# Performance work log

Measured on AMD Instinct MI355X. Metric: run time of the kernel, lower is better.

The kernel has to match this reference:

```python
import jax, jax.numpy as jnp
import numpy as np

D = 1024
H = 16
DH = D // H  # 64
B, S = 4, 1024


def setup_inputs() -> dict:
    key = jax.random.key(0)
    ks = jax.random.split(key, 7)
    sequences = jax.random.normal(ks[0], (B, S, D), dtype=jnp.float32)
    scale = 1.0 / np.sqrt(DH)
    Wq = jax.random.normal(ks[1], (H, DH, DH), dtype=jnp.float32) * scale
    Wk = jax.random.normal(ks[2], (H, DH, DH), dtype=jnp.float32) * scale
    Wv = jax.random.normal(ks[3], (H, DH, DH), dtype=jnp.float32) * scale
    bq = jax.random.normal(ks[4], (H, DH), dtype=jnp.float32) * 0.01
    bk = jax.random.normal(ks[5], (H, DH), dtype=jnp.float32) * 0.01
    bv = jax.random.normal(ks[6], (H, DH), dtype=jnp.float32) * 0.01
    return {"sequences": sequences, "Wq": Wq, "Wk": Wk, "Wv": Wv,
            "bq": bq, "bk": bk, "bv": bv}


def reference(sequences, Wq, Wk, Wv, bq, bk, bv):
    b, s, d = sequences.shape
    x = sequences.reshape(b, s, H, DH)  # split channels into heads
    # per-head Linear: y = x @ W.T + b (torch convention)
    q = jnp.einsum('bshd,hed->bshe', x, Wq) + bq
    k = jnp.einsum('bshd,hed->bshe', x, Wk) + bk
    v = jnp.einsum('bshd,hed->bshe', x, Wv) + bv
    inv_sqrt_dh = jnp.asarray(1.0 / np.sqrt(DH), dtype=sequences.dtype)
    scores = jnp.einsum('bshe,bthe->bhst', q, k) * inv_sqrt_dh  # [B,H,S,S]
    attn = jax.nn.softmax(scores, axis=-1)
    out = jnp.einsum('bhst,bthe->bshe', attn, v)  # [B,S,H,DH]
    return out.reshape(b, s, d)  # hstack of heads == reshape here
```

## Files before the change

kernel.cpp:

```cpp
#include <hip/hip_runtime.h>

#define H 16
#define DH 64
#define BB 4
#define SS 1024
#define DD 1024

typedef __attribute__((ext_vector_type(8))) short bf16x8;
typedef __attribute__((ext_vector_type(4))) float f32x4;
typedef __attribute__((ext_vector_type(4))) unsigned int u32x4;
typedef _Float16 f16x4 __attribute__((ext_vector_type(4)));
typedef _Float16 f16x8 __attribute__((ext_vector_type(8)));
typedef __fp16 hf16x2 __attribute__((ext_vector_type(2)));

#define QSCALE 0.18033688011112042f

#if __has_builtin(__builtin_amdgcn_exp2f)
__device__ __forceinline__ float fast_exp2(float x) {
    return __builtin_amdgcn_exp2f(x);
}
#else
__device__ __forceinline__ float fast_exp2(float x) {
    float r;
    asm("v_exp_f32 %0, %1" : "=v"(r) : "v"(x));
    return r;
}
#endif

__device__ __forceinline__ unsigned short f2bf(float f) {
    union { float f; unsigned u; } v; v.f = f;
    unsigned u = v.u;
    return (unsigned short)((u + 0x7FFFu + ((u >> 16) & 1u)) >> 16);
}

__device__ __forceinline__ unsigned short f2h(float f) {
    union { _Float16 h; unsigned short u; } v;
    v.h = (_Float16)f;
    return v.u;
}

__device__ __forceinline__ void pack8(unsigned short* dst, f32x4 a, f32x4 b) {
    unsigned u0 = (unsigned)f2bf(a[0]) | ((unsigned)f2bf(a[1]) << 16);
    unsigned u1 = (unsigned)f2bf(a[2]) | ((unsigned)f2bf(a[3]) << 16);
    unsigned u2 = (unsigned)f2bf(b[0]) | ((unsigned)f2bf(b[1]) << 16);
    unsigned u3 = (unsigned)f2bf(b[2]) | ((unsigned)f2bf(b[3]) << 16);
    u32x4 v = {u0, u1, u2, u3};
    *(u32x4*)dst = v;
}

__device__ __forceinline__ void async_cp1k(const unsigned short* g,
                                           unsigned short* l, int lane) {
    __builtin_amdgcn_global_load_lds(
        (const __attribute__((address_space(1))) unsigned int*)(g + lane * 8),
        (__attribute__((address_space(3))) unsigned int*)l, 16, 0, 0);
}

__global__ __launch_bounds__(256) void wprep_kernel(
    const float* __restrict__ Wq, const float* __restrict__ Wk,
    const float* __restrict__ Wv, unsigned short* __restrict__ Wp)
{
    const int tg = blockIdx.x * 256 + threadIdx.x;
    const int r = tg >> 2, part = tg & 3;
    const int e = r & 63, hm = r >> 6;
    const int m = hm % 3, h = hm / 3;
    const float* src = (m == 0 ? Wq : (m == 1 ? Wk : Wv)) +
                       (size_t)(h * 64 + e) * 64 + part * 16;
    const float scale = (m == 0) ? QSCALE : 1.0f;
    f32x4 f0 = ((const f32x4*)src)[0];
    f32x4 f1 = ((const f32x4*)src)[1];
    f32x4 f2 = ((const f32x4*)src)[2];
    f32x4 f3 = ((const f32x4*)src)[3];
    f0 *= scale; f1 *= scale; f2 *= scale; f3 *= scale;
    unsigned short tmp[16];
    pack8(tmp, f0, f1);
    pack8(tmp + 8, f2, f3);
    unsigned short* dst = Wp + (size_t)(hm * 64 + e) * 64;
    const int c0 = part * 2, sw = e & 7;
    *(u32x4*)(dst + (c0 ^ sw) * 8)       = *(const u32x4*)tmp;
    *(u32x4*)(dst + ((c0 + 1) ^ sw) * 8) = *(const u32x4*)(tmp + 8);
}

__global__ __launch_bounds__(256) void qkv_kernel(
    const float* __restrict__ x, const unsigned short* __restrict__ Wp,
    const float* __restrict__ bq, const float* __restrict__ bk,
    const float* __restrict__ bv,
    unsigned short* __restrict__ Qg, unsigned short* __restrict__ Kg,
    unsigned short* __restrict__ VTg)
{
    __shared__ __align__(16) unsigned short Xl[4096];
    __shared__ __align__(16) unsigned short Wl[12288];

    const int bid = blockIdx.x;
    const int sc = bid & 15, h = (bid >> 4) & 15, b = bid >> 8;
    const int s0 = sc * 64;
    const int tid = threadIdx.x;
    const int lane = tid & 63, w = tid >> 6;

    {
        const unsigned short* wbase = Wp + (size_t)h * 12288;
#pragma unroll
        for (int sub = 0; sub < 6; sub++) {
            const int off = w * 3072 + sub * 512;
            async_cp1k(wbase + off, &Wl[off], lane);
        }
    }
    {
        const int s = tid >> 2, part = tid & 3;
        const float* src = x + ((size_t)(b * SS + s0 + s)) * DD + h * DH + part * 16;
        f32x4 f0 = ((const f32x4*)src)[0];
        f32x4 f1 = ((const f32x4*)src)[1];
        f32x4 f2 = ((const f32x4*)src)[2];
        f32x4 f3 = ((const f32x4*)src)[3];
        unsigned short tmp[16];
        pack8(tmp, f0, f1);
        pack8(tmp + 8, f2, f3);
        const int c0 = part * 2, sws = s & 7;
        *(u32x4*)&Xl[s * 64 + (c0 ^ sws) * 8]       = *(const u32x4*)tmp;
        *(u32x4*)&Xl[s * 64 + ((c0 + 1) ^ sws) * 8] = *(const u32x4*)(tmp + 8);
    }
    __syncthreads();

    const int l15 = lane & 15, quad = lane >> 4, sw = l15 & 7;

    f32x4 acc[3][4];
#pragma unroll
    for (int m = 0; m < 3; m++)
#pragma unroll
        for (int nt = 0; nt < 4; nt++) acc[m][nt] = (f32x4){0.f, 0.f, 0.f, 0.f};

#pragma unroll
    for (int k2 = 0; k2 < 2; k2++) {
        const int csw = (((k2 << 2) | quad) ^ sw) * 8;
        bf16x8 a = *(const bf16x8*)&Xl[(w * 16 + l15) * 64 + csw];
#pragma unroll
        for (int nt = 0; nt < 4; nt++) {
            const int boff = (nt * 16 + l15) * 64 + csw;
            bf16x8 b0 = *(const bf16x8*)&Wl[boff];
            acc[0][nt] = __builtin_amdgcn_mfma_f32_16x16x32_bf16(a, b0, acc[0][nt], 0, 0, 0);
            bf16x8 b1 = *(const bf16x8*)&Wl[4096 + boff];
            acc[1][nt] = __builtin_amdgcn_mfma_f32_16x16x32_bf16(a, b1, acc[1][nt], 0, 0, 0);
            bf16x8 b2 = *(const bf16x8*)&Wl[8192 + boff];
            acc[2][nt] = __builtin_amdgcn_mfma_f32_16x16x32_bf16(a, b2, acc[2][nt], 0, 0, 0);
        }
    }
    __syncthreads();

#pragma unroll
    for (int nt = 0; nt < 4; nt++) {
        const int e = nt * 16 + l15;
        const float bqs = bq[h * DH + e] * QSCALE;
        const float bks = bk[h * DH + e];
        const float bvs = bv[h * DH + e];
#pragma unroll
        for (int r = 0; r < 4; r++) {
            const int srow = w * 16 + quad * 4 + r;
            Xl[srow * 64 + e] = f2bf(acc[0][nt][r] + bqs);
            Wl[srow * 64 + e] = f2bf(acc[1][nt][r] + bks);
            Wl[4096 + e * 64 + quad * 16 + w * 4 + r] = f2h(acc[2][nt][r] + bvs);
        }
    }
    __syncthreads();
    {
        const size_t bh = (size_t)(b * H + h);
        const int row = tid >> 2, part = tid & 3;
        const int cg = part * 16, c0 = part * 2, swr = row & 7;
        unsigned short* qdst = Qg + (bh * SS + s0 + row) * DH + cg;
        *(u32x4*)qdst       = *(const u32x4*)&Xl[row * 64 + cg];
        *(u32x4*)(qdst + 8) = *(const u32x4*)&Xl[row * 64 + cg + 8];
        unsigned short* kbase = Kg + (bh * 16 + sc) * 4096 + row * 64;
        *(u32x4*)(kbase + (c0 ^ swr) * 8)       = *(const u32x4*)&Wl[row * 64 + c0 * 8];
        *(u32x4*)(kbase + ((c0 + 1) ^ swr) * 8) = *(const u32x4*)&Wl[row * 64 + c0 * 8 + 8];
        unsigned short* vbase = VTg + (bh * 16 + sc) * 4096 + row * 64;
        *(u32x4*)(vbase + (c0 ^ swr) * 8)       = *(const u32x4*)&Wl[4096 + row * 64 + c0 * 8];
        *(u32x4*)(vbase + ((c0 + 1) ^ swr) * 8) = *(const u32x4*)&Wl[4096 + row * 64 + c0 * 8 + 8];
    }
}

__global__ __launch_bounds__(256) void attn_kernel(
    const unsigned short* __restrict__ Qg, const unsigned short* __restrict__ Kg,
    const unsigned short* __restrict__ VTg, float* __restrict__ out)
{
    __shared__ __align__(16) unsigned short Kl0[4096], Kl1[4096];
    __shared__ __align__(16) unsigned short Vl0[4096], Vl1[4096];

    const int bid = blockIdx.x;
    const int bh = bid & 63, qt = bid >> 6;
    const int h = bh & 15, b = bh >> 4;
    const int tid = threadIdx.x;
    const int lane = tid & 63, w = tid >> 6;
    const int l15 = lane & 15, quad = lane >> 4, sw = l15 & 7;

    const unsigned short* Kt = Kg + (size_t)bh * 16 * 4096;
    const unsigned short* Vt = VTg + (size_t)bh * 16 * 4096;

    const int kb0 = l15 * 64 + ((quad)     ^ sw) * 8;
    const int kb1 = l15 * 64 + ((4 | quad) ^ sw) * 8;
    const int vb0 = l15 * 64 + (((quad << 1))     ^ sw) * 8;
    const int vb1 = l15 * 64 + (((quad << 1) | 1) ^ sw) * 8;

    bf16x8 aQ0, aQ1;
    {
        const int qrow = qt * 64 + w * 16 + l15;
        const unsigned short* qp = Qg + ((size_t)bh * SS + qrow) * DH + quad * 8;
        aQ0 = *(const bf16x8*)(qp);
        aQ1 = *(const bf16x8*)(qp + 32);
    }

    {
        const int off = w * 1024;
        async_cp1k(Kt + off,       Kl0 + off,       lane);
        async_cp1k(Kt + off + 512, Kl0 + off + 512, lane);
        async_cp1k(Vt + off,       Vl0 + off,       lane);
        async_cp1k(Vt + off + 512, Vl0 + off + 512, lane);
    }

    f32x4 accO[4];
#pragma unroll
    for (int et = 0; et < 4; et++) accO[et] = (f32x4){0.f, 0.f, 0.f, 0.f};
    float rs_acc = 0.f;

    auto step = [&](int kt, const unsigned short* Kc, const unsigned short* Vc,
                    unsigned short* Kn, unsigned short* Vn) {
        __syncthreads();
        if (kt < 15) {
            const unsigned short* kg = Kt + (kt + 1) * 4096;
            const unsigned short* vg = Vt + (kt + 1) * 4096;
            const int off = w * 1024;
            async_cp1k(kg + off,       Kn + off,       lane);
            async_cp1k(kg + off + 512, Kn + off + 512, lane);
            async_cp1k(vg + off,       Vn + off,       lane);
            async_cp1k(vg + off + 512, Vn + off + 512, lane);
        }

        bf16x8 aK[4][2];
#pragma unroll
        for (int nt = 0; nt < 4; nt++) {
            aK[nt][0] = *(const bf16x8*)(Kc + kb0 + nt * 1024);
            aK[nt][1] = *(const bf16x8*)(Kc + kb1 + nt * 1024);
        }
        f16x8 aV01[4], aV23[4];
#pragma unroll
        for (int et = 0; et < 4; et++) {
            aV01[et] = *(const f16x8*)(Vc + vb0 + et * 1024);
            aV23[et] = *(const f16x8*)(Vc + vb1 + et * 1024);
        }

        f32x4 sc[4];
#pragma unroll
        for (int nt = 0; nt < 4; nt++) {
            f32x4 z = {0.f, 0.f, 0.f, 0.f};
            z = __builtin_amdgcn_mfma_f32_16x16x32_bf16(aK[nt][0], aQ0, z, 0, 0, 0);
            z = __builtin_amdgcn_mfma_f32_16x16x32_bf16(aK[nt][1], aQ1, z, 0, 0, 0);
            sc[nt] = z;
        }

        float rs = 0.f;
        f16x4 pf[4];
#pragma unroll
        for (int nt = 0; nt < 4; nt++) {
            float p0 = fast_exp2(sc[nt][0]);
            float p1 = fast_exp2(sc[nt][1]);
            float p2 = fast_exp2(sc[nt][2]);
            float p3 = fast_exp2(sc[nt][3]);
            rs += (p0 + p1) + (p2 + p3);
            union { hf16x2 h; unsigned u; } lo, hi;
            lo.h = __builtin_amdgcn_cvt_pkrtz(p0, p1);
            hi.h = __builtin_amdgcn_cvt_pkrtz(p2, p3);
            union { unsigned u[2]; f16x4 v; } pk;
            pk.u[0] = lo.u; pk.u[1] = hi.u;
            pf[nt] = pk.v;
        }
        rs_acc += rs;

#pragma unroll
        for (int et = 0; et < 4; et++) {
            f16x4 v0 = __builtin_shufflevector(aV01[et], aV01[et], 0, 1, 2, 3);
            f16x4 v1 = __builtin_shufflevector(aV01[et], aV01[et], 4, 5, 6, 7);
            f16x4 v2 = __builtin_shufflevector(aV23[et], aV23[et], 0, 1, 2, 3);
            f16x4 v3 = __builtin_shufflevector(aV23[et], aV23[et], 4, 5, 6, 7);
            accO[et] = __builtin_amdgcn_mfma_f32_16x16x16f16(v0, pf[0], accO[et], 0, 0, 0);
            accO[et] = __builtin_amdgcn_mfma_f32_16x16x16f16(v1, pf[1], accO[et], 0, 0, 0);
            accO[et] = __builtin_amdgcn_mfma_f32_16x16x16f16(v2, pf[2], accO[et], 0, 0, 0);
            accO[et] = __builtin_amdgcn_mfma_f32_16x16x16f16(v3, pf[3], accO[et], 0, 0, 0);
        }
    };

    for (int i = 0; i < 8; i++) {
        step(2 * i,     Kl0, Vl0, Kl1, Vl1);
        step(2 * i + 1, Kl1, Vl1, Kl0, Vl0);
    }

    {
        float rs = rs_acc;
        rs += __shfl_xor(rs, 16);
        rs += __shfl_xor(rs, 32);
        const float inv = 1.0f / rs;
        const int srow = qt * 64 + w * 16 + l15;
        float* op = out + ((size_t)b * SS + srow) * DD + h * DH;
#pragma unroll
        for (int et = 0; et < 4; et++) {
            f32x4 v = accO[et] * inv;
            *(f32x4*)(op + et * 16 + quad * 4) = v;
        }
    }
}

extern "C" void kernel_launch(void* const* d_in, const int* in_sizes, int n_in,
                              void* d_out, int out_size, void* d_ws, size_t ws_size,
                              hipStream_t stream) {
    const float* x  = (const float*)d_in[0];
    const float* Wq = (const float*)d_in[1];
    const float* Wk = (const float*)d_in[2];
    const float* Wv = (const float*)d_in[3];
    const float* bq = (const float*)d_in[4];
    const float* bk = (const float*)d_in[5];
    const float* bv = (const float*)d_in[6];

    const size_t NE = (size_t)BB * H * SS * DH;
    unsigned short* Qg  = (unsigned short*)d_ws;
    unsigned short* Kg  = Qg + NE;
    unsigned short* VTg = Kg + NE;
    unsigned short* Wp  = VTg + NE;

    wprep_kernel<<<48, 256, 0, stream>>>(Wq, Wk, Wv, Wp);
    qkv_kernel<<<BB * H * (SS / 64), 256, 0, stream>>>(x, Wp, bq, bk, bv,
                                                       Qg, Kg, VTg);
    attn_kernel<<<BB * H * 16, 256, 0, stream>>>(Qg, Kg, VTg, (float*)d_out);
}
```

Before: 119.3 us.

## Split KV sequence across waves with private buffers and cross-wave reduction

```diff
diff --git a/kernel.cpp b/kernel.cpp
--- a/kernel.cpp
+++ b/kernel.cpp
@@ -9,6 +9,7 @@
 typedef __attribute__((ext_vector_type(8))) short bf16x8;
 typedef __attribute__((ext_vector_type(4))) float f32x4;
 typedef __attribute__((ext_vector_type(4))) unsigned int u32x4;
+typedef __attribute__((ext_vector_type(2))) unsigned int u32x2;
 typedef _Float16 f16x4 __attribute__((ext_vector_type(4)));
 typedef _Float16 f16x8 __attribute__((ext_vector_type(8)));
 typedef __fp16 hf16x2 __attribute__((ext_vector_type(2)));
@@ -156,8 +157,13 @@
             const int srow = w * 16 + quad * 4 + r;
             Xl[srow * 64 + e] = f2bf(acc[0][nt][r] + bqs);
             Wl[srow * 64 + e] = f2bf(acc[1][nt][r] + bks);
-            Wl[4096 + e * 64 + quad * 16 + w * 4 + r] = f2h(acc[2][nt][r] + bvs);
-        }
+        }
+        unsigned v01 = (unsigned)f2h(acc[2][nt][0] + bvs) |
+                       ((unsigned)f2h(acc[2][nt][1] + bvs) << 16);
+        unsigned v23 = (unsigned)f2h(acc[2][nt][2] + bvs) |
+                       ((unsigned)f2h(acc[2][nt][3] + bvs) << 16);
+        u32x2 pv = {v01, v23};
+        *(u32x2*)&Wl[4096 + w * 1024 + e * 16 + quad * 4] = pv;
     }
     __syncthreads();
     {
@@ -170,9 +176,9 @@
         unsigned short* kbase = Kg + (bh * 16 + sc) * 4096 + row * 64;
         *(u32x4*)(kbase + (c0 ^ swr) * 8)       = *(const u32x4*)&Wl[row * 64 + c0 * 8];
         *(u32x4*)(kbase + ((c0 + 1) ^ swr) * 8) = *(const u32x4*)&Wl[row * 64 + c0 * 8 + 8];
-        unsigned short* vbase = VTg + (bh * 16 + sc) * 4096 + row * 64;
-        *(u32x4*)(vbase + (c0 ^ swr) * 8)       = *(const u32x4*)&Wl[4096 + row * 64 + c0 * 8];
-        *(u32x4*)(vbase + ((c0 + 1) ^ swr) * 8) = *(const u32x4*)&Wl[4096 + row * 64 + c0 * 8 + 8];
+        unsigned short* vdst = VTg + (bh * 16 + sc) * 4096 + tid * 16;
+        *(u32x4*)vdst       = *(const u32x4*)&Wl[4096 + tid * 16];
+        *(u32x4*)(vdst + 8) = *(const u32x4*)&Wl[4096 + tid * 16 + 8];
     }
 }
 
@@ -180,8 +186,7 @@
     const unsigned short* __restrict__ Qg, const unsigned short* __restrict__ Kg,
     const unsigned short* __restrict__ VTg, float* __restrict__ out)
 {
-    __shared__ __align__(16) unsigned short Kl0[4096], Kl1[4096];
-    __shared__ __align__(16) unsigned short Vl0[4096], Vl1[4096];
+    __shared__ __align__(16) unsigned short L[16384];
 
     const int bid = blockIdx.x;
     const int bh = bid & 63, qt = bid >> 6;
@@ -190,118 +195,125 @@
     const int lane = tid & 63, w = tid >> 6;
     const int l15 = lane & 15, quad = lane >> 4, sw = l15 & 7;
 
-    const unsigned short* Kt = Kg + (size_t)bh * 16 * 4096;
-    const unsigned short* Vt = VTg + (size_t)bh * 16 * 4096;
+    const unsigned short* Kt = Kg + (size_t)bh * 16 * 4096 + w * 1024;
+    const unsigned short* Vt = VTg + (size_t)bh * 16 * 4096 + w * 1024;
+    unsigned short* Lw = &L[w * 4096];
 
     const int kb0 = l15 * 64 + ((quad)     ^ sw) * 8;
     const int kb1 = l15 * 64 + ((4 | quad) ^ sw) * 8;
-    const int vb0 = l15 * 64 + (((quad << 1))     ^ sw) * 8;
-    const int vb1 = l15 * 64 + (((quad << 1) | 1) ^ sw) * 8;
-
-    bf16x8 aQ0, aQ1;
-    {
-        const int qrow = qt * 64 + w * 16 + l15;
-        const unsigned short* qp = Qg + ((size_t)bh * SS + qrow) * DH + quad * 8;
-        aQ0 = *(const bf16x8*)(qp);
-        aQ1 = *(const bf16x8*)(qp + 32);
-    }
-
-    {
-        const int off = w * 1024;
-        async_cp1k(Kt + off,       Kl0 + off,       lane);
-        async_cp1k(Kt + off + 512, Kl0 + off + 512, lane);
-        async_cp1k(Vt + off,       Vl0 + off,       lane);
-        async_cp1k(Vt + off + 512, Vl0 + off + 512, lane);
-    }
-
-    f32x4 accO[4];
-#pragma unroll
-    for (int et = 0; et < 4; et++) accO[et] = (f32x4){0.f, 0.f, 0.f, 0.f};
-    float rs_acc = 0.f;
-
-    auto step = [&](int kt, const unsigned short* Kc, const unsigned short* Vc,
-                    unsigned short* Kn, unsigned short* Vn) {
-        __syncthreads();
-        if (kt < 15) {
-            const unsigned short* kg = Kt + (kt + 1) * 4096;
-            const unsigned short* vg = Vt + (kt + 1) * 4096;
-            const int off = w * 1024;
-            async_cp1k(kg + off,       Kn + off,       lane);
-            async_cp1k(kg + off + 512, Kn + off + 512, lane);
-            async_cp1k(vg + off,       Vn + off,       lane);
-            async_cp1k(vg + off + 512, Vn + off + 512, lane);
-        }
-
-        bf16x8 aK[4][2];
-#pragma unroll
-        for (int nt = 0; nt < 4; nt++) {
-            aK[nt][0] = *(const bf16x8*)(Kc + kb0 + nt * 1024);
-            aK[nt][1] = *(const bf16x8*)(Kc + kb1 + nt * 1024);
-        }
-        f16x8 aV01[4], aV23[4];
-#pragma unroll
-        for (int et = 0; et < 4; et++) {
-            aV01[et] = *(const f16x8*)(Vc + vb0 + et * 1024);
-            aV23[et] = *(const f16x8*)(Vc + vb1 + et * 1024);
-        }
+    const int vb  = 1024 + l15 * 16 + quad * 4;
+
+    bf16x8 aQ0[4], aQ1[4];
+#pragma unroll
+    for (int qb = 0; qb < 4; qb++) {
+        const unsigned short* qp =
+            Qg + ((size_t)bh * SS + qt * 64 + qb * 16 + l15) * DH + quad * 8;
+        aQ0[qb] = *(const bf16x8*)(qp);
+        aQ1[qb] = *(const bf16x8*)(qp + 32);
+    }
+
+    auto stage = [&](int kt, int bufb) {
+        const unsigned short* kg = Kt + kt * 4096;
+        const unsigned short* vg = Vt + kt * 4096;
+        unsigned short* lb = Lw + bufb * 2048;
+        async_cp1k(kg,       lb,        lane);
+        async_cp1k(kg + 512, lb + 512,  lane);
+        async_cp1k(vg,       lb + 1024, lane);
+        async_cp1k(vg + 512, lb + 1536, lane);
+    };
+
+    stage(0, 0);
+    stage(1, 1);
+
+    f32x4 accO[4][4];
+#pragma unroll
+    for (int et = 0; et < 4; et++)
+#pragma unroll
+        for (int qb = 0; qb < 4; qb++) accO[et][qb] = (f32x4){0.f, 0.f, 0.f, 0.f};
+    float rs[4] = {0.f, 0.f, 0.f, 0.f};
+
+#pragma unroll
+    for (int kt = 0; kt < 16; kt++) {
+        if (kt < 15) asm volatile("s_waitcnt vmcnt(4)" ::: "memory");
+        else         asm volatile("s_waitcnt vmcnt(0)" ::: "memory");
+        const unsigned short* Bc = Lw + (kt & 1) * 2048;
+
+        bf16x8 aK0 = *(const bf16x8*)(Bc + kb0);
+        bf16x8 aK1 = *(const bf16x8*)(Bc + kb1);
+        f16x4 aV[4];
+#pragma unroll
+        for (int et = 0; et < 4; et++)
+            aV[et] = *(const f16x4*)(Bc + vb + et * 256);
+        asm volatile("s_waitcnt lgkmcnt(0)" ::: "memory");
+        if (kt < 14) stage(kt + 2, kt & 1);
 
         f32x4 sc[4];
 #pragma unroll
-        for (int nt = 0; nt < 4; nt++) {
+        for (int qb = 0; qb < 4; qb++) {
             f32x4 z = {0.f, 0.f, 0.f, 0.f};
-            z = __builtin_amdgcn_mfma_f32_16x16x32_bf16(aK[nt][0], aQ0, z, 0, 0, 0);
-            z = __builtin_amdgcn_mfma_f32_16x16x32_bf16(aK[nt][1], aQ1, z, 0, 0, 0);
-            sc[nt] = z;
-        }
-
-        float rs = 0.f;
+            z = __builtin_amdgcn_mfma_f32_16x16x32_bf16(aK0, aQ0[qb], z, 0, 0, 0);
+            z = __builtin_amdgcn_mfma_f32_16x16x32_bf16(aK1, aQ1[qb], z, 0, 0, 0);
+            sc[qb] = z;
+        }
+
         f16x4 pf[4];
 #pragma unroll
-        for (int nt = 0; nt < 4; nt++) {
-            float p0 = fast_exp2(sc[nt][0]);
-            float p1 = fast_exp2(sc[nt][1]);
-            float p2 = fast_exp2(sc[nt][2]);
-            float p3 = fast_exp2(sc[nt][3]);
-            rs += (p0 + p1) + (p2 + p3);
+        for (int qb = 0; qb < 4; qb++) {
+            float p0 = fast_exp2(sc[qb][0]);
+            float p1 = fast_exp2(sc[qb][1]);
+            float p2 = fast_exp2(sc[qb][2]);
+            float p3 = fast_exp2(sc[qb][3]);
+            rs[qb] += (p0 + p1) + (p2 + p3);
             union { hf16x2 h; unsigned u; } lo, hi;
             lo.h = __builtin_amdgcn_cvt_pkrtz(p0, p1);
             hi.h = __builtin_amdgcn_cvt_pkrtz(p2, p3);
             union { unsigned u[2]; f16x4 v; } pk;
             pk.u[0] = lo.u; pk.u[1] = hi.u;
-            pf[nt] = pk.v;
-        }
-        rs_acc += rs;
+            pf[qb] = pk.v;
+        }
 
 #pragma unroll
         for (int et = 0; et < 4; et++) {
-            f16x4 v0 = __builtin_shufflevector(aV01[et], aV01[et], 0, 1, 2, 3);
-            f16x4 v1 = __builtin_shufflevector(aV01[et], aV01[et], 4, 5, 6, 7);
-            f16x4 v2 = __builtin_shufflevector(aV23[et], aV23[et], 0, 1, 2, 3);
-            f16x4 v3 = __builtin_shufflevector(aV23[et], aV23[et], 4, 5, 6, 7);
-            accO[et] = __builtin_amdgcn_mfma_f32_16x16x16f16(v0, pf[0], accO[et], 0, 0, 0);
-            accO[et] = __builtin_amdgcn_mfma_f32_16x16x16f16(v1, pf[1], accO[et], 0, 0, 0);
-            accO[et] = __builtin_amdgcn_mfma_f32_16x16x16f16(v2, pf[2], accO[et], 0, 0, 0);
-            accO[et] = __builtin_amdgcn_mfma_f32_16x16x16f16(v3, pf[3], accO[et], 0, 0, 0);
-        }
-    };
-
-    for (int i = 0; i < 8; i++) {
-        step(2 * i,     Kl0, Vl0, Kl1, Vl1);
-        step(2 * i + 1, Kl1, Vl1, Kl0, Vl0);
-    }
-
-    {
-        float rs = rs_acc;
-        rs += __shfl_xor(rs, 16);
-        rs += __shfl_xor(rs, 32);
-        const float inv = 1.0f / rs;
-        const int srow = qt * 64 + w * 16 + l15;
-        float* op = out + ((size_t)b * SS + srow) * DD + h * DH;
-#pragma unroll
-        for (int et = 0; et < 4; et++) {
-            f32x4 v = accO[et] * inv;
-            *(f32x4*)(op + et * 16 + quad * 4) = v;
-        }
+#pragma unroll
+            for (int qb = 0; qb < 4; qb++)
+                accO[et][qb] = __builtin_amdgcn_mfma_f32_16x16x16f16(
+                    aV[et], pf[qb], accO[et][qb], 0, 0, 0);
+        }
+    }
+
+#pragma unroll
+    for (int qb = 0; qb < 4; qb++) {
+        rs[qb] += __shfl_xor(rs[qb], 16);
+        rs[qb] += __shfl_xor(rs[qb], 32);
+    }
+
+    __syncthreads();
+
+    float* R  = (float*)L;
+    float* R2 = (float*)L + 5120;
+    if (quad == 0) {
+#pragma unroll
+        for (int qb = 0; qb < 4; qb++) R2[w * 64 + qb * 16 + l15] = rs[qb];
+    }
+
+    const int q = tid >> 2, eg = tid & 3;
+    float inv = 0.f;
+#pragma unroll
+    for (int et = 0; et < 4; et++) {
+#pragma unroll
+        for (int qb = 0; qb < 4; qb++)
+            *(f32x4*)&R[w * 1280 + (qb * 16 + l15) * 20 + quad * 4] = accO[et][qb];
+        __syncthreads();
+        if (et == 0)
+            inv = 1.0f / (R2[q] + R2[64 + q] + R2[128 + q] + R2[192 + q]);
+        f32x4 o0 = *(const f32x4*)&R[q * 20 + eg * 4];
+        f32x4 o1 = *(const f32x4*)&R[1280 + q * 20 + eg * 4];
+        f32x4 o2 = *(const f32x4*)&R[2560 + q * 20 + eg * 4];
+        f32x4 o3 = *(const f32x4*)&R[3840 + q * 20 + eg * 4];
+        f32x4 o = ((o0 + o1) + (o2 + o3)) * inv;
+        float* op = out + ((size_t)b * SS + qt * 64 + q) * DD + h * DH + et * 16 + eg * 4;
+        *(f32x4*)op = o;
+        if (et < 3) __syncthreads();
     }
 }
 
```

Result: faster. 116.9 us (median of 2 runs) (-2.0%).
